# Performance work log

Measured on AMD Instinct MI355X. Metric: run time of the kernel, lower is better.

The kernel has to match this reference:

```python
import jax, jax.numpy as jnp
import numpy as np

N = 20000      # atom nodes
N_LG = 40000   # line-graph nodes (= undirected bonds)
E = 80000      # directed edges in original graph (= 2*N_LG)
E_LG = 200000  # line-graph edges
L = 5          # num_layer
D = 300        # emb_dim
NUM_ATOM, NUM_BOND, NUM_DIR, NUM_CHI = 120, 6, 3, 3
EPS = 1e-5


def setup_inputs() -> dict:
    key = jax.random.key(0)
    ks = jax.random.split(key, 24)
    ri = lambda k, shape, hi: jax.random.randint(k, shape, 0, hi, dtype=jnp.int32)
    nm = lambda k, shape: jax.random.normal(k, shape, dtype=jnp.float32) * 0.02
    inp = {}
    inp["x"] = ri(ks[0], (N, 2), 3)
    inp["edge_index"] = ri(ks[1], (2, E), N)
    inp["edge_attr"] = ri(ks[2], (E, 2), 3)
    inp["lg_x"] = ri(ks[3], (N_LG, 2), 3)
    inp["lg_edge_index"] = ri(ks[4], (2, E_LG), N_LG)
    inp["lg_edge_index_map"] = ri(ks[5], (2, N_LG), N)
    inp["lg_edge_index_map2"] = ri(ks[6], (E_LG,), N)
    # GNN-level embeddings
    inp["node_emb1"] = nm(ks[7], (NUM_ATOM, D))
    inp["node_emb2"] = nm(ks[8], (NUM_CHI, D))
    inp["gnn_edge_emb1"] = nm(ks[9], (NUM_BOND, D))
    inp["gnn_edge_emb2"] = nm(ks[10], (NUM_DIR, D))
    # per-layer main-graph GINConv params (stacked over layers)
    inp["g_emb1"] = nm(ks[11], (L, NUM_BOND, D))
    inp["g_emb2"] = nm(ks[12], (L, NUM_DIR, D))
    inp["g_w1"] = nm(ks[13], (L, D, 2 * D))
    inp["g_b1"] = jnp.zeros((L, 2 * D), jnp.float32)
    inp["g_w2"] = nm(ks[14], (L, 2 * D, D))
    inp["g_b2"] = jnp.zeros((L, D), jnp.float32)
    inp["g_gamma"] = jnp.ones((L, D), jnp.float32)
    inp["g_beta"] = jnp.zeros((L, D), jnp.float32)
    # per-layer line-graph GINConv params (is_lg=True -> atom/chirality tables)
    inp["lg_emb1"] = nm(ks[15], (L, NUM_ATOM, D))
    inp["lg_emb2"] = nm(ks[16], (L, NUM_CHI, D))
    inp["lg_w1"] = nm(ks[17], (L, D, 2 * D))
    inp["lg_b1"] = jnp.zeros((L, 2 * D), jnp.float32)
    inp["lg_w2"] = nm(ks[18], (L, 2 * D, D))
    inp["lg_b2"] = jnp.zeros((L, D), jnp.float32)
    inp["lg_gamma"] = jnp.ones((L, D), jnp.float32)
    inp["lg_beta"] = jnp.zeros((L, D), jnp.float32)
    return inp


def gin_conv(xn, src, dst, ea, emb1, emb2, sl_idx, w1, b1, w2, b2):
    # self loops appended at the end, with self_loop_attr = emb1[sl_idx] + emb2[0]
    n = xn.shape[0]
    sl = jnp.broadcast_to(emb1[sl_idx] + emb2[0], (n, xn.shape[1]))
    ea_full = jnp.concatenate([ea, sl], axis=0)
    idx = jnp.arange(n, dtype=src.dtype)
    src_f = jnp.concatenate([src, idx])
    dst_f = jnp.concatenate([dst, idx])
    msg = xn[src_f] + ea_full                      # gather + add
    aggr = jax.ops.segment_sum(msg, dst_f, num_segments=n)  # scatter-add
    return jnp.maximum(aggr @ w1 + b1, 0.0) @ w2 + b2        # MLP update


def batchnorm(h, g, b):
    # training-mode BN: batch mean / biased variance (matches torch normalization)
    mu = h.mean(0)
    var = h.var(0)
    return (h - mu) * jax.lax.rsqrt(var + EPS) * g + b


def reference(x, edge_index, edge_attr, lg_x, lg_edge_index, lg_edge_index_map,
              lg_edge_index_map2, node_emb1, node_emb2, gnn_edge_emb1, gnn_edge_emb2,
              g_emb1, g_emb2, g_w1, g_b1, g_w2, g_b2, g_gamma, g_beta,
              lg_emb1, lg_emb2, lg_w1, lg_b1, lg_w2, lg_b2, lg_gamma, lg_beta):
    h = node_emb1[x[:, 0]] + node_emb2[x[:, 1]]
    e = gnn_edge_emb1[lg_x[:, 0]] + gnn_edge_emb2[lg_x[:, 1]]
    h_list, e_list = [h], [e]
    lg_src, lg_dst = lg_edge_index[0], lg_edge_index[1]
    for layer in range(L):
        if layer == 0:
            ea = g_emb1[0][edge_attr[:, 0]] + g_emb2[0][edge_attr[:, 1]]
            src, dst = edge_index[0], edge_index[1]
        else:
            # edge_index rewritten from line-graph map; edge_attr = cat([e, e])
            ea = jnp.concatenate([e_list[layer], e_list[layer]], axis=0)
            src = jnp.concatenate([lg_edge_index_map[0], lg_edge_index_map[1]])
            dst = jnp.concatenate([lg_edge_index_map[1], lg_edge_index_map[0]])
        h = gin_conv(h_list[layer], src, dst, ea, g_emb1[layer], g_emb2[layer], 4,
                     g_w1[layer], g_b1[layer], g_w2[layer], g_b2[layer])
        h = batchnorm(h, g_gamma[layer], g_beta[layer])
        if layer < L - 1:
            h = jnp.maximum(h, 0.0)
        h_list.append(h)
        if layer == 0:
            xa = x[lg_edge_index_map2]  # int atom features of shared node
            lg_ea = lg_emb1[0][xa[:, 0]] + lg_emb2[0][xa[:, 1]]
        else:
            # lg_edge_attr = h[lg_edge_index_map2] from the PREVIOUS iteration's h
            lg_ea = h_list[layer][lg_edge_index_map2]
        e = gin_conv(e_list[layer], lg_src, lg_dst, lg_ea, lg_emb1[layer], lg_emb2[layer], 119,
                     lg_w1[layer], lg_b1[layer], lg_w2[layer], lg_b2[layer])
        e = batchnorm(e, lg_gamma[layer], lg_beta[layer])
        if layer < L - 1:
            e = jnp.maximum(e, 0.0)
        e_list.append(e)
    # (h_list, e_list) packed as one array: [L+1, N + N_LG, D]
    return jnp.concatenate([jnp.stack(h_list), jnp.stack(e_list)], axis=1)
```

## Files before the change

### kernel.cpp

```cpp
#include <hip/hip_runtime.h>

#define D 300

namespace {

constexpr int kN   = 20000;
constexpr int kNLG = 40000;
constexpr int kE   = 80000;
constexpr int kELG = 200000;
constexpr int kL   = 5;

constexpr int K1P = 320;
constexpr int N1P = 640;
constexpr int K2P = 640;
constexpr int N2P = 384;
constexpr int PQH = 320;
constexpr int MP_N   = 20096;
constexpr int MP_ALL = 60160;
constexpr int MAIN_TILES = 157;
constexpr int NRT = 470;
constexpr int NRP = 59;
constexpr int RH = 320;
constexpr int RQ = 40;
constexpr int NALL = kN + kNLG;

typedef __attribute__((ext_vector_type(8))) _Float16 half8;
typedef __attribute__((ext_vector_type(2))) _Float16 half2v;
typedef __attribute__((ext_vector_type(4))) float f32x4;

__device__ inline short f2h(float f) {
  _Float16 h = (_Float16)f;
  return __builtin_bit_cast(short, h);
}

__device__ inline float2 upk(unsigned u) {
  half2v h = __builtin_bit_cast(half2v, u);
  return make_float2((float)h.x, (float)h.y);
}

__device__ inline unsigned pk(float a, float b) {
  half2v h;
  h.x = (_Float16)a;
  h.y = (_Float16)b;
  return __builtin_bit_cast(unsigned, h);
}

__device__ inline void addrow(float* acc, uint4 r) {
  float2 t0 = upk(r.x), t1 = upk(r.y), t2 = upk(r.z), t3 = upk(r.w);
  acc[0] += t0.x; acc[1] += t0.y; acc[2] += t1.x; acc[3] += t1.y;
  acc[4] += t2.x; acc[5] += t2.y; acc[6] += t3.x; acc[7] += t3.y;
}

__device__ inline void unpk8(uint4 r, float* v) {
  float2 t0 = upk(r.x), t1 = upk(r.y), t2 = upk(r.z), t3 = upk(r.w);
  v[0] = t0.x; v[1] = t0.y; v[2] = t1.x; v[3] = t1.y;
  v[4] = t2.x; v[5] = t2.y; v[6] = t3.x; v[7] = t3.y;
}

__device__ inline uint4 pk4(const float* a) {
  uint4 r;
  r.x = pk(a[0], a[1]); r.y = pk(a[2], a[3]);
  r.z = pk(a[4], a[5]); r.w = pk(a[6], a[7]);
  return r;
}

__device__ inline void gload_lds16(const void* g, void* l) {
  __builtin_amdgcn_global_load_lds(
      (const __attribute__((address_space(1))) void*)g,
      (__attribute__((address_space(3))) void*)l, 16, 0, 0);
}


__global__ void k_init(float* __restrict__ stats, short* __restrict__ ab,
                       int* __restrict__ m0_cur, int* __restrict__ mL_cur,
                       int* __restrict__ lg_cur) {
  int g = blockIdx.x * blockDim.x + threadIdx.x;
  if (g < kL * 1200) stats[g] = 0.f;
  int np1 = (MP_N - kN) * K1P;
  int np2 = (MP_ALL - MP_N - kNLG) * K1P;
  if (g < np1) ab[(size_t)kN * K1P + g] = 0;
  if (g < np2) ab[(size_t)(MP_N + kNLG) * K1P + g] = 0;
  if (g < kN) { m0_cur[g] = 0; mL_cur[g] = 0; }
  if (g < kNLG) lg_cur[g] = 0;
}


__global__ void k_hist_all(const int* __restrict__ edge_index,
                           const int* __restrict__ lg_map,
                           const int* __restrict__ lg_ei,
                           const int* __restrict__ eattr,
                           const int* __restrict__ map2,
                           const int* __restrict__ x,
                           int* __restrict__ m0_cur, int* __restrict__ mL_cur,
                           int* __restrict__ lg_cur,
                           int* __restrict__ cam, int* __restrict__ cal) {
  int g = blockIdx.x * blockDim.x + threadIdx.x;
  if (g < kE) {
    atomicAdd(&m0_cur[edge_index[kE + g]], 1);
    cam[g] = eattr[2 * g] * 3 + eattr[2 * g + 1];
    return;
  }
  g -= kE;
  if (g < kNLG) { atomicAdd(&mL_cur[lg_map[kNLG + g]], 1); return; }
  g -= kNLG;
  if (g < kNLG) { atomicAdd(&mL_cur[lg_map[g]], 1); return; }
  g -= kNLG;
  if (g < kELG) {
    atomicAdd(&lg_cur[lg_ei[kELG + g]], 1);
    int a = map2[g];
    cal[g] = x[2 * a] * 3 + x[2 * a + 1];
  }
}

__device__ void scan_one(int* cursor, int* offs, int n) {
  __shared__ int part[256];
  int tid = threadIdx.x;
  int chunk = (n + 255) / 256;
  int s0 = tid * chunk;
  int s1 = min(n, s0 + chunk);
  int sum = 0;
  for (int i = s0; i < s1; ++i) sum += cursor[i];
  part[tid] = sum;
  __syncthreads();
  for (int off = 1; off < 256; off <<= 1) {
    int v = (tid >= off) ? part[tid - off] : 0;
    __syncthreads();
    part[tid] += v;
    __syncthreads();
  }
  int run = (tid == 0) ? 0 : part[tid - 1];
  for (int i = s0; i < s1; ++i) {
    int dv = cursor[i];
    offs[i] = run;
    cursor[i] = run;
    run += dv;
  }
  if (tid == 255) offs[n] = run;
}

__global__ __launch_bounds__(256) void k_scan3(
    int* __restrict__ m0_cur, int* __restrict__ m0_offs,
    int* __restrict__ mL_cur, int* __restrict__ mL_offs,
    int* __restrict__ lg_cur, int* __restrict__ lg_offs) {
  if (blockIdx.x == 0) scan_one(m0_cur, m0_offs, kN);
  else if (blockIdx.x == 1) scan_one(mL_cur, mL_offs, kN);
  else scan_one(lg_cur, lg_offs, kNLG);
}

__global__ void k_fill_all(const int* __restrict__ edge_index,
                           const int* __restrict__ lg_map,
                           const int* __restrict__ lg_ei,
                           int* __restrict__ m0_cur, int* __restrict__ m0_perm,
                           int* __restrict__ mL_cur, int* __restrict__ mL_perm,
                           int* __restrict__ lg_cur, int* __restrict__ lg_perm) {
  int g = blockIdx.x * blockDim.x + threadIdx.x;
  if (g < kE) {
    int pos = atomicAdd(&m0_cur[edge_index[kE + g]], 1);
    m0_perm[pos] = g;
    return;
  }
  g -= kE;
  if (g < kNLG) {
    int pos = atomicAdd(&mL_cur[lg_map[kNLG + g]], 1);
    mL_perm[pos] = g;
    return;
  }
  g -= kNLG;
  if (g < kNLG) {
    int pos = atomicAdd(&mL_cur[lg_map[g]], 1);
    mL_perm[pos] = kNLG + g;
    return;
  }
  g -= kNLG;
  if (g < kELG) {
    int pos = atomicAdd(&lg_cur[lg_ei[kELG + g]], 1);
    lg_perm[pos] = g;
  }
}


__device__ void cvt_w1(const float* W, short* Wt, int g) {
  int per = N1P * K1P;
  int l = g / per, rem = g - l * per;
  int n = rem / K1P, k = rem - n * K1P;
  float v = (n < 2 * D && k < D) ? W[(size_t)l * D * 2 * D + (size_t)k * 2 * D + n] : 0.f;
  Wt[g] = f2h(v);
}

__device__ void cvt_w2(const float* W, short* Wt, int g) {
  int per = N2P * K2P;
  int l = g / per, rem = g - l * per;
  int n = rem / K2P, k = rem - n * K2P;
  float v = (n < D && k < 2 * D) ? W[(size_t)l * 2 * D * D + (size_t)k * D + n] : 0.f;
  Wt[g] = f2h(v);
}

__global__ void k_precomp(const float* __restrict__ g1, const float* __restrict__ g2,
                          const float* __restrict__ l1, const float* __restrict__ l2,
                          const float* __restrict__ g_w1, const float* __restrict__ g_w2,
                          const float* __restrict__ lg_w1, const float* __restrict__ lg_w2,
                          float* __restrict__ slv, short* __restrict__ tcm,
                          short* __restrict__ tcl,
                          short* __restrict__ g_w1t, short* __restrict__ g_w2t,
                          short* __restrict__ lg_w1t, short* __restrict__ lg_w2t) {
  int g = blockIdx.x * blockDim.x + threadIdx.x;
  const int s1 = kL * N1P * K1P, s2 = kL * N2P * K2P;
  if (g < s1) { cvt_w1(g_w1, g_w1t, g); return; }
  g -= s1;
  if (g < s2) { cvt_w2(g_w2, g_w2t, g); return; }
  g -= s2;
  if (g < s1) { cvt_w1(lg_w1, lg_w1t, g); return; }
  g -= s1;
  if (g < s2) { cvt_w2(lg_w2, lg_w2t, g); return; }
  g -= s2;
  if (g < kL * 640) {
    int l = g / 640, rem = g - l * 640;
    int gr = rem / 320, c = rem - gr * 320;
    float v = 0.f;
    if (c < D) {
      if (gr == 0) v = g1[(size_t)l * 6 * D + 4 * D + c] + g2[(size_t)l * 3 * D + c];
      else         v = l1[(size_t)l * 120 * D + 119 * D + c] + l2[(size_t)l * 3 * D + c];
    }
    slv[g] = v;
    return;
  }
  g -= kL * 640;
  if (g < 18 * RH) {
    int p = g / RH, c = g - p * RH;
    float v = (c < D) ? g1[(size_t)(p / 3) * D + c] + g2[(size_t)(p % 3) * D + c] : 0.f;
    tcm[g] = f2h(v);
    return;
  }
  g -= 18 * RH;
  if (g < 360 * RH) {
    int p = g / RH, c = g - p * RH;
    float v = (c < D) ? l1[(size_t)(p / 3) * D + c] + l2[(size_t)(p % 3) * D + c] : 0.f;
    tcl[g] = f2h(v);
  }
}


__global__ void k_embed_all(const int* __restrict__ x, const int* __restrict__ lg_x,
                            const float* __restrict__ t1m, const float* __restrict__ t2m,
                            const float* __restrict__ t1l, const float* __restrict__ t2l,
                            float* __restrict__ outF, uint4* __restrict__ hist) {
  int g = blockIdx.x * blockDim.x + threadIdx.x;
  if (g >= NALL * RQ) return;
  int r = g / RQ, q = g - r * RQ;
  bool m = r < kN;
  int i = m ? r : r - kN;
  const int* ix = (m ? x : lg_x) + 2 * i;
  const float* t1 = (m ? t1m : t1l) + (size_t)ix[0] * D;
  const float* t2 = (m ? t2m : t2l) + (size_t)ix[1] * D;
  int c0 = q * 8;
  float y[8] = {0.f, 0.f, 0.f, 0.f, 0.f, 0.f, 0.f, 0.f};
  if (c0 < D) {
    float4 p0 = *(const float4*)(t1 + c0);
    float4 q0 = *(const float4*)(t2 + c0);
    y[0] = p0.x + q0.x; y[1] = p0.y + q0.y; y[2] = p0.z + q0.z; y[3] = p0.w + q0.w;
    *(float4*)(outF + (size_t)r * D + c0) = make_float4(y[0], y[1], y[2], y[3]);
    if (c0 + 8 <= D) {
      float4 p1 = *(const float4*)(t1 + c0 + 4);
      float4 q1 = *(const float4*)(t2 + c0 + 4);
      y[4] = p1.x + q1.x; y[5] = p1.y + q1.y; y[6] = p1.z + q1.z; y[7] = p1.w + q1.w;
      *(float4*)(outF + (size_t)r * D + c0 + 4) = make_float4(y[4], y[5], y[6], y[7]);
    }
  }
  hist[(size_t)r * RQ + q] = pk4(y);
}


#define GATHER_BODY                                                     \
  int p0 = offs[j], p1 = offs[j + 1];                                   \
  for (int pb = p0; pb < p1; pb += 64) {                                \
    int cnt = min(64, p1 - pb);                                         \
    int e_ = permp[pb + ((lane < cnt) ? lane : 0)];                     \
    int ra, rb;                                                         \
    GATHER_IDX                                                          \
    int t = 0;                                                          \
    for (; t + 3 < cnt; t += 4) {                                       \
      int a0 = __shfl(ra, t),     b0 = __shfl(rb, t);                   \
      int a1 = __shfl(ra, t + 1), b1 = __shfl(rb, t + 1);               \
      int a2 = __shfl(ra, t + 2), b2 = __shfl(rb, t + 2);               \
      int a3 = __shfl(ra, t + 3), b3 = __shfl(rb, t + 3);               \
      uint4 x0 = bA[(size_t)a0 * RQ + ll];                              \
      uint4 y0 = bB[(size_t)b0 * RQ + ll];                              \
      uint4 x1 = bA[(size_t)a1 * RQ + ll];                              \
      uint4 y1 = bB[(size_t)b1 * RQ + ll];                              \
      uint4 x2 = bA[(size_t)a2 * RQ + ll];                              \
      uint4 y2 = bB[(size_t)b2 * RQ + ll];                              \
      uint4 x3 = bA[(size_t)a3 * RQ + ll];                              \
      uint4 y3 = bB[(size_t)b3 * RQ + ll];                              \
      addrow(acc, x0); addrow(acc, y0);                                 \
      addrow(acc, x1); addrow(acc, y1);                                 \
      addrow(acc, x2); addrow(acc, y2);                                 \
      addrow(acc, x3); addrow(acc, y3);                                 \
    }                                                                   \
    for (; t < cnt; ++t) {                                              \
      int a0 = __shfl(ra, t), b0 = __shfl(rb, t);                       \
      uint4 x0 = bA[(size_t)a0 * RQ + ll];                              \
      uint4 y0 = bB[(size_t)b0 * RQ + ll];                              \
      addrow(acc, x0); addrow(acc, y0);                                 \
    }                                                                   \
  }

__global__ __launch_bounds__(64) void k_gather_all0(
    const uint4* __restrict__ h16, const uint4* __restrict__ e16,
    const int* __restrict__ m_src, const int* __restrict__ lg_src,
    const int* __restrict__ cam, const int* __restrict__ cal,
    const uint4* __restrict__ tcm, const uint4* __restrict__ tcl,
    const float* __restrict__ slvM, const float* __restrict__ slvL,
    const int* __restrict__ m_offs, const int* __restrict__ m_perm,
    const int* __restrict__ l_offs, const int* __restrict__ l_perm,
    uint4* __restrict__ ab) {
  int node = blockIdx.x;
  int lane = threadIdx.x;
  bool act = lane < RQ;
  int ll = act ? lane : 0;
  bool isM = node < kN;
  int j = isM ? node : node - kN;
  const uint4* selfrow = isM ? (h16 + (size_t)node * RQ) : (e16 + (size_t)j * RQ);
  const float* sv = (isM ? slvM : slvL) + ll * 8;
  const int* offs = isM ? m_offs : l_offs;
  const int* permp = isM ? m_perm : l_perm;
  const uint4* bA = isM ? h16 : e16;
  const uint4* bB = isM ? tcm : tcl;
  const int* srcp = isM ? m_src : lg_src;
  const int* catp = isM ? cam : cal;

  float acc[8];
  {
    float vv[8];
    unpk8(selfrow[ll], vv);
#pragma unroll
    for (int i = 0; i < 8; ++i) acc[i] = vv[i] + sv[i];
  }

#define GATHER_IDX ra = srcp[e_]; rb = catp[e_];
  GATHER_BODY
#undef GATHER_IDX

  if (act) ab[(size_t)(isM ? node : MP_N + j) * RQ + ll] = pk4(acc);
}

__global__ __launch_bounds__(64) void k_gather_allL(
    const uint4* __restrict__ h16, const uint4* __restrict__ e16,
    const int* __restrict__ lg_map, const int* __restrict__ lg_src,
    const int* __restrict__ map2,
    const float* __restrict__ slvM, const float* __restrict__ slvL,
    const int* __restrict__ m_offs, const int* __restrict__ m_perm,
    const int* __restrict__ l_offs, const int* __restrict__ l_perm,
    uint4* __restrict__ ab) {
  int node = blockIdx.x;
  int lane = threadIdx.x;
  bool act = lane < RQ;
  int ll = act ? lane : 0;
  bool isM = node < kN;
  int j = isM ? node : node - kN;
  const uint4* selfrow = isM ? (h16 + (size_t)node * RQ) : (e16 + (size_t)j * RQ);
  const float* sv = (isM ? slvM : slvL) + ll * 8;
  const int* offs = isM ? m_offs : l_offs;
  const int* permp = isM ? m_perm : l_perm;
  const uint4* bA = isM ? h16 : e16;
  const uint4* bB = isM ? e16 : h16;

  float acc[8];
  {
    float vv[8];
    unpk8(selfrow[ll], vv);
#pragma unroll
    for (int i = 0; i < 8; ++i) acc[i] = vv[i] + sv[i];
  }

#define GATHER_IDX                                     \
  if (isM) {                                           \
    ra = lg_map[e_];                                   \
    rb = (e_ < kNLG) ? e_ : e_ - kNLG;                 \
  } else {                                             \
    ra = lg_src[e_];                                   \
    rb = map2[e_];                                     \
  }
  GATHER_BODY
#undef GATHER_IDX

  if (act) ab[(size_t)(isM ? node : MP_N + j) * RQ + ll] = pk4(acc);
}


template<bool RELU, bool STATS>
__global__ __launch_bounds__(256) void k_mfma_gemm_dual(
    const short* __restrict__ A,
    const short* __restrict__ BtM, const short* __restrict__ BtL,
    const float* __restrict__ biasM, const float* __restrict__ biasL, int biasN,
    short* __restrict__ Cout, int Cstat, int Cwrite, int Cstride,
    int Astride, int Kloop, int NC,
    int mainLimit, int lgLimit,
    float* __restrict__ statsM, float* __restrict__ statsL) {
  __shared__ __align__(16) short ldsA[2][128 * 32];
  __shared__ __align__(16) short ldsB[2][128 * 32];
  __shared__ float sd[256];

  int bid = blockIdx.x;
  int xcd = bid & 7;
  int t0 = bid >> 3;
  int c = t0 % NC;
  int rr = t0 / NC;
  int rtile = rr * 8 + xcd;
  if (rtile >= NRT) return;

  const int tid = threadIdx.x;
  const int lane = tid & 63, w = tid >> 6;
  const bool isMain = rtile < MAIN_TILES;
  const short* Bt = isMain ? BtM : BtL;
  const float* bias = isMain ? biasM : biasL;
  const int rowLimit = isMain ? mainLimit : lgLimit;
  const int brow = rtile * 128;
  const int bcol = c * 128;
  const int wr = w >> 1, wc = w & 1;

  if (STATS) sd[tid] = 0.f;

  f32x4 acc[4][4] = {};

  const int sr = tid >> 2;
  const int sc = (tid & 3) * 8;

  auto stage = [&](int buf, int k0) {
    char* la = (char*)(&ldsA[buf][0]) + w * 1024;
    char* lb = (char*)(&ldsB[buf][0]) + w * 1024;
    const short* gA0 = A + (size_t)(brow + sr) * Astride + (k0 + sc);
    const short* gB0 = Bt + (size_t)(bcol + sr) * Astride + (k0 + sc);
    gload_lds16(gA0, la);
    gload_lds16(gA0 + (size_t)64 * Astride, la + 4096);
    gload_lds16(gB0, lb);
    gload_lds16(gB0 + (size_t)64 * Astride, lb + 4096);
  };

  const int nt = Kloop / 32;
  stage(0, 0);
  __syncthreads();

  for (int t = 0; t < nt; ++t) {
    int cb = t & 1;
    if (t + 1 < nt) stage(cb ^ 1, (t + 1) * 32);

    const int kq = (lane >> 4) * 16;
    const char* baseA = (const char*)(&ldsA[cb][0]);
    const char* baseB = (const char*)(&ldsB[cb][0]);
    half8 af[4], bf[4];
#pragma unroll
    for (int m = 0; m < 4; ++m) {
      int row = wr * 64 + m * 16 + (lane & 15);
      af[m] = *(const half8*)(baseA + row * 64 + kq);
    }
#pragma unroll
    for (int n = 0; n < 4; ++n) {
      int col = wc * 64 + n * 16 + (lane & 15);
      bf[n] = *(const half8*)(baseB + col * 64 + kq);
    }
#pragma unroll
    for (int m = 0; m < 4; ++m)
#pragma unroll
      for (int n = 0; n < 4; ++n)
        acc[m][n] = __builtin_amdgcn_mfma_f32_16x16x32_f16(af[m], bf[n], acc[m][n], 0, 0, 0);
    __syncthreads();
  }

  const int r0 = brow + wr * 64;
  const int c0 = bcol + wc * 64;
  float ps[4] = {}, pq[4] = {};
#pragma unroll
  for (int m = 0; m < 4; ++m) {
#pragma unroll
    for (int i = 0; i < 4; ++i) {
      int row = r0 + m * 16 + (lane >> 4) * 4 + i;
      bool rv = row < rowLimit;
#pragma unroll
      for (int n = 0; n < 4; ++n) {
        int col = c0 + n * 16 + (lane & 15);
        float bv = (col < biasN) ? bias[col] : 0.f;
        float v = acc[m][n][i] + bv;
        if (RELU) v = fmaxf(v, 0.f);
        if (rv && col < Cwrite) {
          Cout[(size_t)row * Cstride + col] = f2h(v);
          if (STATS && col < Cstat) { ps[n] += v; pq[n] += v * v; }
        }
      }
    }
  }

  if (STATS) {
#pragma unroll
    for (int n = 0; n < 4; ++n) {
      float s = ps[n], q = pq[n];
      s += __shfl_xor(s, 16); q += __shfl_xor(q, 16);
      s += __shfl_xor(s, 32); q += __shfl_xor(q, 32);
      if ((lane >> 4) == 0) {
        int cc = wc * 64 + n * 16 + (lane & 15);
        atomicAdd(&sd[cc], s);
        atomicAdd(&sd[128 + cc], q);
      }
    }
    __syncthreads();
    float* gs = isMain ? statsM : statsL;
    if (tid < 128) {
      int col = bcol + tid;
      if (col < Cstat) {
        atomicAdd(&gs[col], sd[tid]);
        atomicAdd(&gs[D + col], sd[128 + tid]);
      }
    }
  }
}


__global__ void k_bn_coef(const float* __restrict__ stats,
                          const float* __restrict__ gM, const float* __restrict__ bM,
                          const float* __restrict__ gL, const float* __restrict__ bL,
                          float* __restrict__ coef) {
  int t = blockIdx.x * blockDim.x + threadIdx.x;
  if (t >= 640) return;
  bool m = t < 320;
  int c = m ? t : t - 320;
  float a = 0.f, b = 0.f;
  if (c < D) {
    const float* s = stats + (m ? 0 : 600);
    float inv_n = m ? (1.f / kN) : (1.f / kNLG);
    float mu = s[c] * inv_n;
    float var = s[D + c] * inv_n - mu * mu;
    a = rsqrtf(var + 1e-5f) * (m ? gM : gL)[c];
    b = (m ? bM : bL)[c] - mu * a;
  }
  int base = m ? 0 : 640;
  coef[base + c] = a;
  coef[base + 320 + c] = b;
}


template<bool RELU, bool WRITE_HIST>
__global__ void k_bn_apply_v(const uint4* __restrict__ pre, const float* __restrict__ coef,
                             float* __restrict__ outF, uint4* __restrict__ hist) {
  int g = blockIdx.x * blockDim.x + threadIdx.x;
  if (g >= NALL * RQ) return;
  int r = g / RQ, q = g - r * RQ;
  bool m = r < kN;
  int pr = m ? r : MP_N + (r - kN);
  float v[8], y[8];
  unpk8(pre[(size_t)pr * RQ + q], v);
  const float* cb = coef + (m ? 0 : 640);
  float4 a0 = *(const float4*)(cb + q * 8);
  float4 a1 = *(const float4*)(cb + q * 8 + 4);
  float4 b0 = *(const float4*)(cb + 320 + q * 8);
  float4 b1 = *(const float4*)(cb + 320 + q * 8 + 4);
  y[0] = a0.x * v[0] + b0.x; y[1] = a0.y * v[1] + b0.y;
  y[2] = a0.z * v[2] + b0.z; y[3] = a0.w * v[3] + b0.w;
  y[4] = a1.x * v[4] + b1.x; y[5] = a1.y * v[5] + b1.y;
  y[6] = a1.z * v[6] + b1.z; y[7] = a1.w * v[7] + b1.w;
  if (RELU) {
#pragma unroll
    for (int i = 0; i < 8; ++i) y[i] = fmaxf(y[i], 0.f);
  }
  float* op = outF + (size_t)r * D + q * 8;
  if (q < 37) {
    *(float4*)op = make_float4(y[0], y[1], y[2], y[3]);
    *(float4*)(op + 4) = make_float4(y[4], y[5], y[6], y[7]);
  } else if (q == 37) {
    *(float4*)op = make_float4(y[0], y[1], y[2], y[3]);
  }
  if (WRITE_HIST) hist[(size_t)r * RQ + q] = pk4(y);
}

}

extern "C" void kernel_launch(void* const* d_in, const int* in_sizes, int n_in,
                              void* d_out_v, int out_size, void* d_ws, size_t ws_size,
                              hipStream_t stream) {
  const int*   x            = (const int*)d_in[0];
  const int*   edge_index   = (const int*)d_in[1];
  const int*   edge_attr    = (const int*)d_in[2];
  const int*   lg_x         = (const int*)d_in[3];
  const int*   lg_edge_index= (const int*)d_in[4];
  const int*   lg_map       = (const int*)d_in[5];
  const int*   lg_map2      = (const int*)d_in[6];
  const float* node_emb1    = (const float*)d_in[7];
  const float* node_emb2    = (const float*)d_in[8];
  const float* gnn_e_emb1   = (const float*)d_in[9];
  const float* gnn_e_emb2   = (const float*)d_in[10];
  const float* g_emb1       = (const float*)d_in[11];
  const float* g_emb2       = (const float*)d_in[12];
  const float* g_w1         = (const float*)d_in[13];
  const float* g_b1         = (const float*)d_in[14];
  const float* g_w2         = (const float*)d_in[15];
  const float* g_b2         = (const float*)d_in[16];
  const float* g_gamma      = (const float*)d_in[17];
  const float* g_beta       = (const float*)d_in[18];
  const float* lg_emb1      = (const float*)d_in[19];
  const float* lg_emb2      = (const float*)d_in[20];
  const float* lg_w1        = (const float*)d_in[21];
  const float* lg_b1        = (const float*)d_in[22];
  const float* lg_w2        = (const float*)d_in[23];
  const float* lg_b2        = (const float*)d_in[24];
  const float* lg_gamma     = (const float*)d_in[25];
  const float* lg_beta      = (const float*)d_in[26];

  float* out = (float*)d_out_v;
  char*  ws  = (char*)d_ws;

  size_t off = 0;
  auto alloc = [&](size_t bytes) { void* p = ws + off; off = (off + bytes + 255) & ~(size_t)255; return p; };
  short* ab      = (short*)alloc((size_t)MP_ALL * K1P * 2);
  short* hidden  = (short*)alloc((size_t)MP_ALL * N1P * 2);
  short* pre16   = (short*)alloc((size_t)MP_ALL * PQH * 2);
  short* hist2   = (short*)alloc((size_t)2 * NALL * RH * 2);
  short* g_w1t   = (short*)alloc((size_t)kL * N1P * K1P * 2);
  short* g_w2t   = (short*)alloc((size_t)kL * N2P * K2P * 2);
  short* lg_w1t  = (short*)alloc((size_t)kL * N1P * K1P * 2);
  short* lg_w2t  = (short*)alloc((size_t)kL * N2P * K2P * 2);
  float* stats   = (float*)alloc(kL * 1200 * 4);
  float* slv     = (float*)alloc(kL * 640 * 4);
  float* coef    = (float*)alloc(1280 * 4);
  short* tcm     = (short*)alloc(18 * RH * 2);
  short* tcl     = (short*)alloc(360 * RH * 2);
  int* cam     = (int*)alloc(kE * 4);
  int* cal     = (int*)alloc(kELG * 4);
  int* m0_offs = (int*)alloc((kN + 1) * 4);
  int* m0_cur  = (int*)alloc(kN * 4);
  int* m0_perm = (int*)alloc(kE * 4);
  int* mL_offs = (int*)alloc((kN + 1) * 4);
  int* mL_cur  = (int*)alloc(kN * 4);
  int* mL_perm = (int*)alloc(2 * kNLG * 4);
  int* lg_offs = (int*)alloc((kNLG + 1) * 4);
  int* lg_cur  = (int*)alloc(kNLG * 4);
  int* lg_perm = (int*)alloc(kELG * 4);

  auto hptr = [&](int l) { return out + (size_t)l * 60000 * D; };
  auto slot_h = [&](int s) { return hist2 + (size_t)s * NALL * RH; };
  auto slot_e = [&](int s) { return hist2 + (size_t)s * NALL * RH + (size_t)kN * RH; };

  dim3 b(256);

  k_init<<<(kNLG + 255) / 256, b, 0, stream>>>(stats, ab, m0_cur, mL_cur, lg_cur);
  {
    int tot = kE + 2 * kNLG + kELG;
    k_hist_all<<<(tot + 255) / 256, b, 0, stream>>>(edge_index, lg_map, lg_edge_index,
                                                    edge_attr, lg_map2, x,
                                                    m0_cur, mL_cur, lg_cur, cam, cal);
    k_scan3<<<3, b, 0, stream>>>(m0_cur, m0_offs, mL_cur, mL_offs, lg_cur, lg_offs);
    k_fill_all<<<(tot + 255) / 256, b, 0, stream>>>(edge_index, lg_map, lg_edge_index,
                                                    m0_cur, m0_perm, mL_cur, mL_perm,
                                                    lg_cur, lg_perm);
  }
  {
    int tot = 2 * kL * (N1P * K1P + N2P * K2P) + kL * 640 + 378 * RH;
    k_precomp<<<(tot + 255) / 256, b, 0, stream>>>(g_emb1, g_emb2, lg_emb1, lg_emb2,
                                                   g_w1, g_w2, lg_w1, lg_w2,
                                                   slv, tcm, tcl,
                                                   g_w1t, g_w2t, lg_w1t, lg_w2t);
  }
  k_embed_all<<<(NALL * RQ + 255) / 256, b, 0, stream>>>(x, lg_x, node_emb1, node_emb2,
                                                         gnn_e_emb1, gnn_e_emb2,
                                                         hptr(0), (uint4*)slot_h(0));

  int cur = 0;
  for (int l = 0; l < kL; ++l) {
    float* slot = stats + (size_t)l * 1200;
    const float* slvM = slv + (size_t)l * 640;
    const float* slvL = slvM + 320;

    if (l == 0)
      k_gather_all0<<<NALL, 64, 0, stream>>>(
          (const uint4*)slot_h(cur), (const uint4*)slot_e(cur),
          edge_index, lg_edge_index, cam, cal,
          (const uint4*)tcm, (const uint4*)tcl,
          slvM, slvL, m0_offs, m0_perm, lg_offs, lg_perm, (uint4*)ab);
    else
      k_gather_allL<<<NALL, 64, 0, stream>>>(
          (const uint4*)slot_h(cur), (const uint4*)slot_e(cur),
          lg_map, lg_edge_index, lg_map2,
          slvM, slvL, mL_offs, mL_perm, lg_offs, lg_perm, (uint4*)ab);

    k_mfma_gemm_dual<true, false><<<8 * NRP * 5, b, 0, stream>>>(
        ab, g_w1t + (size_t)l * N1P * K1P, lg_w1t + (size_t)l * N1P * K1P,
        g_b1 + (size_t)l * 2 * D, lg_b1 + (size_t)l * 2 * D, 2 * D,
        hidden, 0, 608, N1P, K1P, K1P, 5, MP_ALL, MP_ALL, nullptr, nullptr);

    k_mfma_gemm_dual<false, true><<<8 * NRP * 3, b, 0, stream>>>(
        hidden, g_w2t + (size_t)l * N2P * K2P, lg_w2t + (size_t)l * N2P * K2P,
        g_b2 + (size_t)l * D, lg_b2 + (size_t)l * D, D,
        pre16, D, PQH, PQH, K2P, 608, 3, kN, MP_N + kNLG,
        slot, slot + 600);

    k_bn_coef<<<3, b, 0, stream>>>(slot,
                                   g_gamma + (size_t)l * D, g_beta + (size_t)l * D,
                                   lg_gamma + (size_t)l * D, lg_beta + (size_t)l * D, coef);

    int nxt = cur ^ 1;
    if (l < kL - 1)
      k_bn_apply_v<true, true><<<(NALL * RQ + 255) / 256, b, 0, stream>>>(
          (const uint4*)pre16, coef, hptr(l + 1), (uint4*)slot_h(nxt));
    else
      k_bn_apply_v<false, false><<<(NALL * RQ + 255) / 256, b, 0, stream>>>(
          (const uint4*)pre16, coef, hptr(l + 1), (uint4*)slot_h(nxt));
    cur = nxt;
  }
}
```

Baseline: 1.389 ms.

## Fuse batchnorm+ReLU apply into the next layer's neighbor gather

Drops the separate BN-apply pass that wrote normalized bf16 history rows. The next layer's gather now reads the raw pre-BN GEMM output, applies the BN scale/shift and ReLU to every gathered row on the fly, and writes the fp32 layer output from its self-row. A final BN kernel still runs for the last layer. This saves a full read/write pass per layer at the cost of extra FMA/ReLU work per gathered row and a double-buffered pre-activation array.

New measurement: 1.344 ms. 1.03x faster.

```diff
diff --git a/kernel.cpp b/kernel.cpp
--- a/kernel.cpp
+++ b/kernel.cpp
@@ -270,40 +270,6 @@
 }
 
 
-#define GATHER_BODY                                                     \
-  int p0 = offs[j], p1 = offs[j + 1];                                   \
-  for (int pb = p0; pb < p1; pb += 64) {                                \
-    int cnt = min(64, p1 - pb);                                         \
-    int e_ = permp[pb + ((lane < cnt) ? lane : 0)];                     \
-    int ra, rb;                                                         \
-    GATHER_IDX                                                          \
-    int t = 0;                                                          \
-    for (; t + 3 < cnt; t += 4) {                                       \
-      int a0 = __shfl(ra, t),     b0 = __shfl(rb, t);                   \
-      int a1 = __shfl(ra, t + 1), b1 = __shfl(rb, t + 1);               \
-      int a2 = __shfl(ra, t + 2), b2 = __shfl(rb, t + 2);               \
-      int a3 = __shfl(ra, t + 3), b3 = __shfl(rb, t + 3);               \
-      uint4 x0 = bA[(size_t)a0 * RQ + ll];                              \
-      uint4 y0 = bB[(size_t)b0 * RQ + ll];                              \
-      uint4 x1 = bA[(size_t)a1 * RQ + ll];                              \
-      uint4 y1 = bB[(size_t)b1 * RQ + ll];                              \
-      uint4 x2 = bA[(size_t)a2 * RQ + ll];                              \
-      uint4 y2 = bB[(size_t)b2 * RQ + ll];                              \
-      uint4 x3 = bA[(size_t)a3 * RQ + ll];                              \
-      uint4 y3 = bB[(size_t)b3 * RQ + ll];                              \
-      addrow(acc, x0); addrow(acc, y0);                                 \
-      addrow(acc, x1); addrow(acc, y1);                                 \
-      addrow(acc, x2); addrow(acc, y2);                                 \
-      addrow(acc, x3); addrow(acc, y3);                                 \
-    }                                                                   \
-    for (; t < cnt; ++t) {                                              \
-      int a0 = __shfl(ra, t), b0 = __shfl(rb, t);                       \
-      uint4 x0 = bA[(size_t)a0 * RQ + ll];                              \
-      uint4 y0 = bB[(size_t)b0 * RQ + ll];                              \
-      addrow(acc, x0); addrow(acc, y0);                                 \
-    }                                                                   \
-  }
-
 __global__ __launch_bounds__(64) void k_gather_all0(
     const uint4* __restrict__ h16, const uint4* __restrict__ e16,
     const int* __restrict__ m_src, const int* __restrict__ lg_src,
@@ -336,53 +302,143 @@
     for (int i = 0; i < 8; ++i) acc[i] = vv[i] + sv[i];
   }
 
-#define GATHER_IDX ra = srcp[e_]; rb = catp[e_];
-  GATHER_BODY
-#undef GATHER_IDX
-
+  int p0 = offs[j], p1 = offs[j + 1];
+  for (int pb = p0; pb < p1; pb += 64) {
+    int cnt = min(64, p1 - pb);
+    int e_ = permp[pb + ((lane < cnt) ? lane : 0)];
+    int ra = srcp[e_], rb = catp[e_];
+    int t = 0;
+    for (; t + 3 < cnt; t += 4) {
+      int a0 = __shfl(ra, t),     b0 = __shfl(rb, t);
+      int a1 = __shfl(ra, t + 1), b1 = __shfl(rb, t + 1);
+      int a2 = __shfl(ra, t + 2), b2 = __shfl(rb, t + 2);
+      int a3 = __shfl(ra, t + 3), b3 = __shfl(rb, t + 3);
+      uint4 x0 = bA[(size_t)a0 * RQ + ll];
+      uint4 y0 = bB[(size_t)b0 * RQ + ll];
+      uint4 x1 = bA[(size_t)a1 * RQ + ll];
+      uint4 y1 = bB[(size_t)b1 * RQ + ll];
+      uint4 x2 = bA[(size_t)a2 * RQ + ll];
+      uint4 y2 = bB[(size_t)b2 * RQ + ll];
+      uint4 x3 = bA[(size_t)a3 * RQ + ll];
+      uint4 y3 = bB[(size_t)b3 * RQ + ll];
+      addrow(acc, x0); addrow(acc, y0);
+      addrow(acc, x1); addrow(acc, y1);
+      addrow(acc, x2); addrow(acc, y2);
+      addrow(acc, x3); addrow(acc, y3);
+    }
+    for (; t < cnt; ++t) {
+      int a0 = __shfl(ra, t), b0 = __shfl(rb, t);
+      uint4 x0 = bA[(size_t)a0 * RQ + ll];
+      uint4 y0 = bB[(size_t)b0 * RQ + ll];
+      addrow(acc, x0); addrow(acc, y0);
+    }
+  }
   if (act) ab[(size_t)(isM ? node : MP_N + j) * RQ + ll] = pk4(acc);
 }
 
-__global__ __launch_bounds__(64) void k_gather_allL(
-    const uint4* __restrict__ h16, const uint4* __restrict__ e16,
+
+__global__ __launch_bounds__(64) void k_gather_bnL(
+    const uint4* __restrict__ pre, const float* __restrict__ coef,
     const int* __restrict__ lg_map, const int* __restrict__ lg_src,
     const int* __restrict__ map2,
     const float* __restrict__ slvM, const float* __restrict__ slvL,
     const int* __restrict__ m_offs, const int* __restrict__ m_perm,
     const int* __restrict__ l_offs, const int* __restrict__ l_perm,
-    uint4* __restrict__ ab) {
+    float* __restrict__ outF, uint4* __restrict__ ab) {
   int node = blockIdx.x;
   int lane = threadIdx.x;
   bool act = lane < RQ;
   int ll = act ? lane : 0;
   bool isM = node < kN;
   int j = isM ? node : node - kN;
-  const uint4* selfrow = isM ? (h16 + (size_t)node * RQ) : (e16 + (size_t)j * RQ);
+
+  float aM[8], bM[8], aL[8], bL[8];
+  {
+    float4 t;
+    t = *(const float4*)(coef + ll * 8);            aM[0]=t.x; aM[1]=t.y; aM[2]=t.z; aM[3]=t.w;
+    t = *(const float4*)(coef + ll * 8 + 4);        aM[4]=t.x; aM[5]=t.y; aM[6]=t.z; aM[7]=t.w;
+    t = *(const float4*)(coef + 320 + ll * 8);      bM[0]=t.x; bM[1]=t.y; bM[2]=t.z; bM[3]=t.w;
+    t = *(const float4*)(coef + 320 + ll * 8 + 4);  bM[4]=t.x; bM[5]=t.y; bM[6]=t.z; bM[7]=t.w;
+    t = *(const float4*)(coef + 640 + ll * 8);      aL[0]=t.x; aL[1]=t.y; aL[2]=t.z; aL[3]=t.w;
+    t = *(const float4*)(coef + 640 + ll * 8 + 4);  aL[4]=t.x; aL[5]=t.y; aL[6]=t.z; aL[7]=t.w;
+    t = *(const float4*)(coef + 960 + ll * 8);      bL[0]=t.x; bL[1]=t.y; bL[2]=t.z; bL[3]=t.w;
+    t = *(const float4*)(coef + 960 + ll * 8 + 4);  bL[4]=t.x; bL[5]=t.y; bL[6]=t.z; bL[7]=t.w;
+  }
+
   const float* sv = (isM ? slvM : slvL) + ll * 8;
   const int* offs = isM ? m_offs : l_offs;
   const int* permp = isM ? m_perm : l_perm;
-  const uint4* bA = isM ? h16 : e16;
-  const uint4* bB = isM ? e16 : h16;
 
   float acc[8];
   {
-    float vv[8];
-    unpk8(selfrow[ll], vv);
-#pragma unroll
-    for (int i = 0; i < 8; ++i) acc[i] = vv[i] + sv[i];
-  }
-
-#define GATHER_IDX                                     \
-  if (isM) {                                           \
-    ra = lg_map[e_];                                   \
-    rb = (e_ < kNLG) ? e_ : e_ - kNLG;                 \
-  } else {                                             \
-    ra = lg_src[e_];                                   \
-    rb = map2[e_];                                     \
-  }
-  GATHER_BODY
-#undef GATHER_IDX
-
+    int selfIdx = isM ? node : MP_N + j;
+    float vv[8], y[8];
+    unpk8(pre[(size_t)selfIdx * RQ + ll], vv);
+#pragma unroll
+    for (int i = 0; i < 8; ++i) {
+      float a = isM ? aM[i] : aL[i];
+      float b = isM ? bM[i] : bL[i];
+      y[i] = fmaxf(a * vv[i] + b, 0.f);
+      acc[i] = y[i] + sv[i];
+    }
+    if (act) {
+      float* op = outF + (size_t)node * D + ll * 8;
+      if (ll < 37) {
+        *(float4*)op = make_float4(y[0], y[1], y[2], y[3]);
+        *(float4*)(op + 4) = make_float4(y[4], y[5], y[6], y[7]);
+      } else if (ll == 37) {
+        *(float4*)op = make_float4(y[0], y[1], y[2], y[3]);
+      }
+    }
+  }
+
+  int p0 = offs[j], p1 = offs[j + 1];
+  for (int pb = p0; pb < p1; pb += 64) {
+    int cnt = min(64, p1 - pb);
+    int e_ = permp[pb + ((lane < cnt) ? lane : 0)];
+    int rh, re;
+    if (isM) {
+      rh = lg_map[e_];
+      re = MP_N + ((e_ < kNLG) ? e_ : e_ - kNLG);
+    } else {
+      rh = map2[e_];
+      re = MP_N + lg_src[e_];
+    }
+    int t = 0;
+    for (; t + 1 < cnt; t += 2) {
+      int h0 = __shfl(rh, t),     e0 = __shfl(re, t);
+      int h1 = __shfl(rh, t + 1), e1 = __shfl(re, t + 1);
+      uint4 xh0 = pre[(size_t)h0 * RQ + ll];
+      uint4 xe0 = pre[(size_t)e0 * RQ + ll];
+      uint4 xh1 = pre[(size_t)h1 * RQ + ll];
+      uint4 xe1 = pre[(size_t)e1 * RQ + ll];
+      float v[8];
+      unpk8(xh0, v);
+#pragma unroll
+      for (int i = 0; i < 8; ++i) acc[i] += fmaxf(aM[i] * v[i] + bM[i], 0.f);
+      unpk8(xe0, v);
+#pragma unroll
+      for (int i = 0; i < 8; ++i) acc[i] += fmaxf(aL[i] * v[i] + bL[i], 0.f);
+      unpk8(xh1, v);
+#pragma unroll
+      for (int i = 0; i < 8; ++i) acc[i] += fmaxf(aM[i] * v[i] + bM[i], 0.f);
+      unpk8(xe1, v);
+#pragma unroll
+      for (int i = 0; i < 8; ++i) acc[i] += fmaxf(aL[i] * v[i] + bL[i], 0.f);
+    }
+    if (t < cnt) {
+      int h0 = __shfl(rh, t), e0 = __shfl(re, t);
+      uint4 xh0 = pre[(size_t)h0 * RQ + ll];
+      uint4 xe0 = pre[(size_t)e0 * RQ + ll];
+      float v[8];
+      unpk8(xh0, v);
+#pragma unroll
+      for (int i = 0; i < 8; ++i) acc[i] += fmaxf(aM[i] * v[i] + bM[i], 0.f);
+      unpk8(xe0, v);
+#pragma unroll
+      for (int i = 0; i < 8; ++i) acc[i] += fmaxf(aL[i] * v[i] + bL[i], 0.f);
+    }
+  }
   if (act) ab[(size_t)(isM ? node : MP_N + j) * RQ + ll] = pk4(acc);
 }
 
@@ -537,9 +593,8 @@
 }
 
 
-template<bool RELU, bool WRITE_HIST>
-__global__ void k_bn_apply_v(const uint4* __restrict__ pre, const float* __restrict__ coef,
-                             float* __restrict__ outF, uint4* __restrict__ hist) {
+__global__ void k_bn_final(const uint4* __restrict__ pre, const float* __restrict__ coef,
+                           float* __restrict__ outF) {
   int g = blockIdx.x * blockDim.x + threadIdx.x;
   if (g >= NALL * RQ) return;
   int r = g / RQ, q = g - r * RQ;
@@ -556,10 +611,6 @@
   y[2] = a0.z * v[2] + b0.z; y[3] = a0.w * v[3] + b0.w;
   y[4] = a1.x * v[4] + b1.x; y[5] = a1.y * v[5] + b1.y;
   y[6] = a1.z * v[6] + b1.z; y[7] = a1.w * v[7] + b1.w;
-  if (RELU) {
-#pragma unroll
-    for (int i = 0; i < 8; ++i) y[i] = fmaxf(y[i], 0.f);
-  }
   float* op = outF + (size_t)r * D + q * 8;
   if (q < 37) {
     *(float4*)op = make_float4(y[0], y[1], y[2], y[3]);
@@ -567,7 +618,6 @@
   } else if (q == 37) {
     *(float4*)op = make_float4(y[0], y[1], y[2], y[3]);
   }
-  if (WRITE_HIST) hist[(size_t)r * RQ + q] = pk4(y);
 }
 
 }
@@ -610,13 +660,13 @@
   auto alloc = [&](size_t bytes) { void* p = ws + off; off = (off + bytes + 255) & ~(size_t)255; return p; };
   short* ab      = (short*)alloc((size_t)MP_ALL * K1P * 2);
   short* hidden  = (short*)alloc((size_t)MP_ALL * N1P * 2);
-  short* pre16   = (short*)alloc((size_t)MP_ALL * PQH * 2);
-  short* hist2   = (short*)alloc((size_t)2 * NALL * RH * 2);
+  short* pre2    = (short*)alloc((size_t)2 * MP_ALL * PQH * 2);
+  short* hist    = (short*)alloc((size_t)NALL * RH * 2);
   short* g_w1t   = (short*)alloc((size_t)kL * N1P * K1P * 2);
   short* g_w2t   = (short*)alloc((size_t)kL * N2P * K2P * 2);
   short* lg_w1t  = (short*)alloc((size_t)kL * N1P * K1P * 2);
   short* lg_w2t  = (short*)alloc((size_t)kL * N2P * K2P * 2);
-  float* stats   = (float*)alloc(kL * 1200 * 4);
+  float* stats   = (float*)alloc((kL * 1200 + 64) * 4);
   float* slv     = (float*)alloc(kL * 640 * 4);
   float* coef    = (float*)alloc(1280 * 4);
   short* tcm     = (short*)alloc(18 * RH * 2);
@@ -634,8 +684,7 @@
   int* lg_perm = (int*)alloc(kELG * 4);
 
   auto hptr = [&](int l) { return out + (size_t)l * 60000 * D; };
-  auto slot_h = [&](int s) { return hist2 + (size_t)s * NALL * RH; };
-  auto slot_e = [&](int s) { return hist2 + (size_t)s * NALL * RH + (size_t)kN * RH; };
+  auto prep = [&](int s) { return pre2 + (size_t)s * MP_ALL * PQH; };
 
   dim3 b(256);
 
@@ -659,7 +708,7 @@
   }
   k_embed_all<<<(NALL * RQ + 255) / 256, b, 0, stream>>>(x, lg_x, node_emb1, node_emb2,
                                                          gnn_e_emb1, gnn_e_emb2,
-                                                         hptr(0), (uint4*)slot_h(0));
+                                                         hptr(0), (uint4*)hist);
 
   int cur = 0;
   for (int l = 0; l < kL; ++l) {
@@ -669,38 +718,34 @@
 
     if (l == 0)
       k_gather_all0<<<NALL, 64, 0, stream>>>(
-          (const uint4*)slot_h(cur), (const uint4*)slot_e(cur),
+          (const uint4*)hist, (const uint4*)(hist + (size_t)kN * RH),
           edge_index, lg_edge_index, cam, cal,
           (const uint4*)tcm, (const uint4*)tcl,
           slvM, slvL, m0_offs, m0_perm, lg_offs, lg_perm, (uint4*)ab);
     else
-      k_gather_allL<<<NALL, 64, 0, stream>>>(
-          (const uint4*)slot_h(cur), (const uint4*)slot_e(cur),
-          lg_map, lg_edge_index, lg_map2,
-          slvM, slvL, mL_offs, mL_perm, lg_offs, lg_perm, (uint4*)ab);
+      k_gather_bnL<<<NALL, 64, 0, stream>>>(
+          (const uint4*)prep(cur), coef, lg_map, lg_edge_index, lg_map2,
+          slvM, slvL, mL_offs, mL_perm, lg_offs, lg_perm,
+          hptr(l), (uint4*)ab);
 
     k_mfma_gemm_dual<true, false><<<8 * NRP * 5, b, 0, stream>>>(
         ab, g_w1t + (size_t)l * N1P * K1P, lg_w1t + (size_t)l * N1P * K1P,
         g_b1 + (size_t)l * 2 * D, lg_b1 + (size_t)l * 2 * D, 2 * D,
         hidden, 0, 608, N1P, K1P, K1P, 5, MP_ALL, MP_ALL, nullptr, nullptr);
 
+    int nxt = cur ^ 1;
     k_mfma_gemm_dual<false, true><<<8 * NRP * 3, b, 0, stream>>>(
         hidden, g_w2t + (size_t)l * N2P * K2P, lg_w2t + (size_t)l * N2P * K2P,
         g_b2 + (size_t)l * D, lg_b2 + (size_t)l * D, D,
-        pre16, D, PQH, PQH, K2P, 608, 3, kN, MP_N + kNLG,
+        prep(nxt), D, PQH, PQH, K2P, 608, 3, kN, MP_N + kNLG,
         slot, slot + 600);
 
     k_bn_coef<<<3, b, 0, stream>>>(slot,
                                    g_gamma + (size_t)l * D, g_beta + (size_t)l * D,
                                    lg_gamma + (size_t)l * D, lg_beta + (size_t)l * D, coef);
-
-    int nxt = cur ^ 1;
-    if (l < kL - 1)
-      k_bn_apply_v<true, true><<<(NALL * RQ + 255) / 256, b, 0, stream>>>(
-          (const uint4*)pre16, coef, hptr(l + 1), (uint4*)slot_h(nxt));
-    else
-      k_bn_apply_v<false, false><<<(NALL * RQ + 255) / 256, b, 0, stream>>>(
-          (const uint4*)pre16, coef, hptr(l + 1), (uint4*)slot_h(nxt));
     cur = nxt;
   }
-}
+
+  k_bn_final<<<(NALL * RQ + 255) / 256, b, 0, stream>>>(
+      (const uint4*)prep(cur), coef, hptr(kL));
+}
```
